# Optimization experiments

Measured on AMD Instinct MI355X. Metric: run time of the kernel, lower is better.

Reference implementation:

```python
import jax, jax.numpy as jnp
import numpy as np

SEQ_LEN = 2048   # configs.seq_len == h == KFSSM H
PRED_LEN = 720   # configs.pred_len == p
D_MODEL = 128    # configs.d_model == KFSSM N (complex state size N//2)
C_OUT = 64       # configs.c_out == channel dim of u
BATCH = 128


def setup_inputs() -> dict:
    key = jax.random.key(0)
    ks = jax.random.split(key, 12)
    H, n2, p = SEQ_LEN, D_MODEL // 2, PRED_LEN
    u = jax.random.normal(ks[0], (BATCH, SEQ_LEN, C_OUT), jnp.float32)
    x_mark_enc = jax.random.normal(ks[1], (BATCH, SEQ_LEN, 4), jnp.float32)
    x_dec = jax.random.normal(ks[2], (BATCH, PRED_LEN, C_OUT), jnp.float32)
    x_mark_dec = jax.random.normal(ks[3], (BATCH, PRED_LEN, 4), jnp.float32)
    # standard-normal noise; scaled by learned std inside reference (matches torch.normal(0, std))
    W_noise = jax.random.normal(ks[4], (BATCH, SEQ_LEN, C_OUT), jnp.float32)
    # Model params
    D = jax.random.normal(ks[5], (H,), jnp.float32)
    log_variance = jnp.log(1.0 + jax.random.uniform(ks[6], (1,), jnp.float32))
    # KFSSM params
    C_param = jax.random.normal(ks[7], (H, n2, 2), jnp.float32)  # view_as_real of complex C
    log_dt = (jax.random.uniform(ks[8], (H,), jnp.float32)
              * (np.log(0.1) - np.log(0.001)) + np.log(0.001))
    log_A_real = jnp.log(0.5 * jnp.ones((H, n2), jnp.float32))
    A_imag = np.pi * jnp.tile(jnp.arange(n2, dtype=jnp.float32)[None, :], (H, 1))
    # outporj: Linear(h -> 2p) then GLU(dim=2)
    proj_w = jax.random.normal(ks[9], (2 * p, H), jnp.float32) * 0.02
    proj_b = jnp.zeros((2 * p,), jnp.float32)
    return dict(u=u, x_mark_enc=x_mark_enc, x_dec=x_dec, x_mark_dec=x_mark_dec,
                W_noise=W_noise, D=D, log_variance=log_variance, C_param=C_param,
                log_dt=log_dt, log_A_real=log_A_real, A_imag=A_imag,
                proj_w=proj_w, proj_b=proj_b)


def _ssm_kernels(Nl, C_param, log_dt, log_A_real, A_imag):
    # KFSSM.forward(N=Nl): returns K, K2 of shape (H, Nl)
    dt = jnp.exp(log_dt)                              # (H,)
    C = C_param[..., 0] + 1j * C_param[..., 1]        # (H, n2)
    A = -jnp.exp(log_A_real) + 1j * A_imag            # (H, n2)
    ar = jnp.arange(Nl, dtype=log_dt.dtype)
    Bk = A[:, :1] * ar[None, :] * dt[:, None]         # (H, Nl) complex
    dtA = A * dt[:, None]                             # (H, n2)
    Kexp = jnp.exp(dtA[:, :, None] * ar[None, None, :])  # (H, n2, Nl)
    Cc = C * (jnp.exp(dtA) - 1.0) / A                 # (H, n2)
    K = 2.0 * jnp.einsum('hn,hnl->hl', Cc, Kexp).real # (H, Nl)
    K2 = 2.0 * (K * Bk).real                          # (H, Nl)
    return K, K2


def reference(u, x_mark_enc, x_dec, x_mark_dec, W_noise, D, log_variance,
              C_param, log_dt, log_A_real, A_imag, proj_w, proj_b):
    # instance normalization over time
    x_mean = jnp.mean(u, axis=1, keepdims=True)                  # (B,1,N)
    u0 = u - x_mean
    x_var = jnp.var(u0, axis=1, ddof=1, keepdims=True) + 1e-5    # unbiased, as torch.var
    un = u0 / jnp.sqrt(x_var)
    # Kalman process noise
    std = jnp.sqrt(jnp.exp(log_variance))                        # (1,)
    W = std * W_noise                                            # (B,L,N)
    l, Nch = un.shape[1], un.shape[2]
    nfft = 2 * l
    K, K2 = _ssm_kernels(Nch, C_param, log_dt, log_A_real, A_imag)  # (H=l, Nch)
    k_f = jnp.fft.rfft(K.T, n=nfft, axis=-1)                     # (Nch, l+1)
    k2_f = jnp.fft.rfft(K2.T, n=nfft, axis=-1)
    u_f = jnp.fft.rfft(jnp.transpose(un, (0, 2, 1)), n=nfft, axis=-1)   # (B,Nch,l+1)
    w_f = jnp.fft.rfft(jnp.transpose(W, (0, 2, 1)), n=nfft, axis=-1)
    y = (jnp.fft.irfft(u_f * k2_f, n=nfft, axis=-1)
         + jnp.fft.irfft(w_f * k_f, n=nfft, axis=-1))            # (B,Nch,2l)
    y = jnp.transpose(y, (0, 2, 1))[:, -l:, :] + un * D[:, None] # (B,l,Nch)
    # outporj: Linear(h->2p) over time axis, then GLU(dim=2); Dropout1d is identity at eval
    z = jnp.einsum('bnh,ph->bnp', jnp.transpose(y, (0, 2, 1)), proj_w) + proj_b  # (B,Nch,2p)
    a, b = jnp.split(z, 2, axis=2)
    y = jnp.transpose(a * jax.nn.sigmoid(b), (0, 2, 1))          # (B,p,Nch)
    y = y * jnp.sqrt(x_var) + x_mean
    return y[:, -PRED_LEN:, :]
```

## Files before the change

kernel.cpp:

```cpp
#include <hip/hip_runtime.h>
#include <math.h>

typedef unsigned short u16;
typedef unsigned int u32;
typedef __attribute__((ext_vector_type(8))) short short8;
typedef __attribute__((ext_vector_type(4))) float f32x4;

#define B_   128
#define L_   2048
#define C_   64
#define P_   720
#define P2_  1440
#define NPAD 1536
#define NFFT 4096
#define NROW (B_*C_)
#define TCHUNK 16

#define PREP_SSMK   512
#define PREP_STATS1 2048
#define PREP_NB     (PREP_SSMK + PREP_STATS1 + 1 + (NPAD * L_) / 256)
#define PF_PACK  4096
#define PF_FFTK  64
#define PF_NB    (PF_PACK + PF_FFTK + 32)

__device__ __forceinline__ u16 f2bf(float f) {
  union { float f; unsigned u; } x; x.f = f;
  unsigned r = x.u + 0x7fffu + ((x.u >> 16) & 1u);
  return (u16)(r >> 16);
}
__device__ __forceinline__ float bf2f_lo(u32 v) {
  union { unsigned u; float f; } x; x.u = v << 16; return x.f;
}
__device__ __forceinline__ float bf2f_hi(u32 v) {
  union { unsigned u; float f; } x; x.u = v & 0xffff0000u; return x.f;
}

__device__ __forceinline__ float2 cmul(float2 a, float2 b) {
  return make_float2(a.x * b.x - a.y * b.y, a.x * b.y + a.y * b.x);
}
__device__ __forceinline__ float2 cadd(float2 a, float2 b) { return make_float2(a.x + b.x, a.y + b.y); }
__device__ __forceinline__ float2 csub(float2 a, float2 b) { return make_float2(a.x - b.x, a.y - b.y); }

#define CSWAP(i, j) { float2 tt = a[i]; a[i] = a[j]; a[j] = tt; }

template<bool INV, bool HZ>
__device__ __forceinline__ void dft16(float2 a[16]) {
  const float S  = INV ? 1.f : -1.f;
  const float c1 = 0.9238795325112867f, s1 = 0.3826834323650898f, q2 = 0.7071067811865476f;
  const float2 W1 = make_float2( c1, S * s1), W2 = make_float2( q2, S * q2), W3 = make_float2( s1, S * c1);
  const float2 W5 = make_float2(-s1, S * c1), W6 = make_float2(-q2, S * q2), W7 = make_float2(-c1, S * s1);
  if (HZ) {
    a[8]  = a[0];
    a[9]  = cmul(a[1], W1);
    a[10] = cmul(a[2], W2);
    a[11] = cmul(a[3], W3);
    a[12] = make_float2(-S * a[4].y, S * a[4].x);
    a[13] = cmul(a[5], W5);
    a[14] = cmul(a[6], W6);
    a[15] = cmul(a[7], W7);
  } else {
    float2 t;
    t = csub(a[0], a[8]);  a[0] = cadd(a[0], a[8]);  a[8]  = t;
    t = csub(a[1], a[9]);  a[1] = cadd(a[1], a[9]);  a[9]  = cmul(t, W1);
    t = csub(a[2], a[10]); a[2] = cadd(a[2], a[10]); a[10] = cmul(t, W2);
    t = csub(a[3], a[11]); a[3] = cadd(a[3], a[11]); a[11] = cmul(t, W3);
    t = csub(a[4], a[12]); a[4] = cadd(a[4], a[12]); a[12] = make_float2(-S * t.y, S * t.x);
    t = csub(a[5], a[13]); a[5] = cadd(a[5], a[13]); a[13] = cmul(t, W5);
    t = csub(a[6], a[14]); a[6] = cadd(a[6], a[14]); a[14] = cmul(t, W6);
    t = csub(a[7], a[15]); a[7] = cadd(a[7], a[15]); a[15] = cmul(t, W7);
  }
#pragma unroll
  for (int h = 0; h < 16; h += 8) {
    float2 t;
    t = csub(a[h+0], a[h+4]); a[h+0] = cadd(a[h+0], a[h+4]); a[h+4] = t;
    t = csub(a[h+1], a[h+5]); a[h+1] = cadd(a[h+1], a[h+5]); a[h+5] = cmul(t, W2);
    t = csub(a[h+2], a[h+6]); a[h+2] = cadd(a[h+2], a[h+6]); a[h+6] = make_float2(-S * t.y, S * t.x);
    t = csub(a[h+3], a[h+7]); a[h+3] = cadd(a[h+3], a[h+7]); a[h+7] = cmul(t, W6);
  }
#pragma unroll
  for (int q = 0; q < 16; q += 4) {
    float2 t;
    t = csub(a[q+0], a[q+2]); a[q+0] = cadd(a[q+0], a[q+2]); a[q+2] = t;
    t = csub(a[q+1], a[q+3]); a[q+1] = cadd(a[q+1], a[q+3]); a[q+3] = make_float2(-S * t.y, S * t.x);
  }
#pragma unroll
  for (int p = 0; p < 16; p += 2) {
    float2 t = csub(a[p], a[p+1]); a[p] = cadd(a[p], a[p+1]); a[p+1] = t;
  }
  CSWAP(1, 8); CSWAP(2, 4); CSWAP(3, 12); CSWAP(5, 10); CSWAP(7, 14); CSWAP(11, 13);
}

__device__ __forceinline__ void twchain(float2 a[16], float2 w1) {
  float2 w2 = cmul(w1, w1);
  float2 w3 = cmul(w2, w1);
  float2 w4 = cmul(w2, w2);
  float2 w5 = cmul(w3, w2);
  float2 w6 = cmul(w3, w3);
  float2 w7 = cmul(w4, w3);
  float2 w8 = cmul(w4, w4);
  float2 w9 = cmul(w5, w4);
  float2 w10 = cmul(w5, w5);
  float2 w11 = cmul(w6, w5);
  float2 w12 = cmul(w6, w6);
  float2 w13 = cmul(w7, w6);
  float2 w14 = cmul(w7, w7);
  float2 w15 = cmul(w8, w7);
  a[1]  = cmul(a[1],  w1);  a[2]  = cmul(a[2],  w2);  a[3]  = cmul(a[3],  w3);
  a[4]  = cmul(a[4],  w4);  a[5]  = cmul(a[5],  w5);  a[6]  = cmul(a[6],  w6);
  a[7]  = cmul(a[7],  w7);  a[8]  = cmul(a[8],  w8);  a[9]  = cmul(a[9],  w9);
  a[10] = cmul(a[10], w10); a[11] = cmul(a[11], w11); a[12] = cmul(a[12], w12);
  a[13] = cmul(a[13], w13); a[14] = cmul(a[14], w14); a[15] = cmul(a[15], w15);
}

__device__ __forceinline__ void lds_wA(float2* X, const float2 r[16], int tid) {
  int base = (tid & 15) * 16 + ((tid >> 4) ^ ((tid & 7) << 1));
#pragma unroll
  for (int i = 0; i < 16; ++i) X[base + i * 256] = r[i];
}
__device__ __forceinline__ void lds_wB(float2* X, const float2 r[16], int tid) {
#pragma unroll
  for (int i = 0; i < 16; ++i)
    X[((tid & 0xF0) + i) * 16 + ((tid & 15) ^ ((i & 7) << 1))] = r[i];
}
__device__ __forceinline__ void lds_rd(const float2* X, float2 r[16], int tid) {
  const float4* X4 = (const float4*)X;
#pragma unroll
  for (int p = 0; p < 8; ++p) {
    float4 v = X4[tid * 8 + (p ^ (tid & 7))];
    r[2 * p]     = make_float2(v.x, v.y);
    r[2 * p + 1] = make_float2(v.z, v.w);
  }
}

__device__ __forceinline__ void fft_fwd_hz(float2 r[16], float2* X, int tid, const float2* twg) {
  dft16<false, true>(r);
  twchain(r, twg[tid]);
  lds_wA(X, r, tid);
  __syncthreads();
  lds_rd(X, r, tid);
  dft16<false, false>(r);
  twchain(r, twg[(tid & 15) << 4]);
  __syncthreads();
  lds_wB(X, r, tid);
  __syncthreads();
  lds_rd(X, r, tid);
  dft16<false, false>(r);
}

__device__ __forceinline__ void fft_inv(float2 r[16], float2* X, int tid, const float2* twg) {
  dft16<true, false>(r);
  __syncthreads();
  lds_wB(X, r, tid);
  __syncthreads();
  lds_rd(X, r, tid);
  float2 wb = twg[(tid & 15) << 4];
  twchain(r, make_float2(wb.x, -wb.y));
  dft16<true, false>(r);
  __syncthreads();
  lds_wA(X, r, tid);
  __syncthreads();
  lds_rd(X, r, tid);
  float2 wa = twg[tid];
  twchain(r, make_float2(wa.x, -wa.y));
  dft16<true, false>(r);
}

__global__ __launch_bounds__(256) void k_prep(const float* __restrict__ pw, u16* __restrict__ wb,
                                              const float* __restrict__ u, float* __restrict__ ps,
                                              float* __restrict__ pq,
                                              const float* __restrict__ Cp, const float* __restrict__ ldt,
                                              const float* __restrict__ lAr, const float* __restrict__ Aim,
                                              float2* __restrict__ kz, float2* __restrict__ tw) {
  __shared__ float4 sb[16][16], qb[16][16];
  int blk = blockIdx.x, tid = threadIdx.x;
  if (blk < PREP_SSMK) {
    int gid = blk * 256 + tid;
    int h = gid & 2047;
    int j = gid >> 11;
    float dt = expf(ldt[h]);
    float accx = 0.f;
    float Ar0 = 0.f;
    for (int n = 0; n < 64; ++n) {
      float Ar = -expf(lAr[h * 64 + n]);
      float Ai = Aim[h * 64 + n];
      if (n == 0) Ar0 = Ar;
      float dAr = Ar * dt, dAi = Ai * dt;
      float er = expf(dAr);
      float s1, c1; sincosf(dAi, &s1, &c1);
      float emr = er * c1 - 1.0f, emi = er * s1;
      float inv = 1.0f / (Ar * Ar + Ai * Ai);
      float qr = (emr * Ar + emi * Ai) * inv;
      float qi = (emi * Ar - emr * Ai) * inv;
      float cr = Cp[(size_t)(h * 64 + n) * 2];
      float ci = Cp[(size_t)(h * 64 + n) * 2 + 1];
      float ccr = cr * qr - ci * qi;
      float cci = cr * qi + ci * qr;
      float ej = expf(dAr * (float)j);
      float sj, cj; sincosf(dAi * (float)j, &sj, &cj);
      accx += ccr * (ej * cj) - cci * (ej * sj);
    }
    float K = 2.0f * accx;
    float K2 = 2.0f * K * (Ar0 * (float)j * dt);
    kz[(size_t)j * L_ + h] = make_float2(K2, -K);
  } else if (blk < PREP_SSMK + PREP_STATS1) {
    int blk2 = blk - PREP_SSMK;
    int b = blk2 >> 4, q = blk2 & 15;
    int c4 = tid & 15, g = tid >> 4;
    const float4* u4 = (const float4*)(u + ((size_t)b * L_ + q * 128) * C_);
    float4 s = make_float4(0.f, 0.f, 0.f, 0.f), sq = s;
#pragma unroll
    for (int i = 0; i < 8; ++i) {
      float4 v = u4[(size_t)(g + 16 * i) * 16 + c4];
      s.x += v.x; s.y += v.y; s.z += v.z; s.w += v.w;
      sq.x += v.x * v.x; sq.y += v.y * v.y; sq.z += v.z * v.z; sq.w += v.w * v.w;
    }
    sb[g][c4] = s; qb[g][c4] = sq;
    __syncthreads();
    if (g == 0) {
      float4 S = sb[0][c4], Q = qb[0][c4];
#pragma unroll
      for (int k = 1; k < 16; ++k) {
        float4 a = sb[k][c4], d = qb[k][c4];
        S.x += a.x; S.y += a.y; S.z += a.z; S.w += a.w;
        Q.x += d.x; Q.y += d.y; Q.z += d.z; Q.w += d.w;
      }
      ((float4*)ps)[blk2 * 16 + c4] = S;
      ((float4*)pq)[blk2 * 16 + c4] = Q;
    }
  } else if (blk == PREP_SSMK + PREP_STATS1) {
    int k = tid;
    double ang = -2.0 * 3.14159265358979323846 * (double)k / 4096.0;
    tw[k] = make_float2((float)cos(ang), (float)sin(ang));
  } else {
    size_t idx = (size_t)(blk - (PREP_SSMK + PREP_STATS1 + 1)) * 256 + tid;
    int n = (int)(idx >> 11);
    int k = (int)(idx & 2047);
    int q = n >> 1;
    float v = 0.f;
    if (q < P_) {
      int p = (n & 1) ? (P_ + q) : q;
      v = pw[(size_t)p * L_ + k];
    }
    wb[idx] = f2bf(v);
  }
}

__global__ __launch_bounds__(256) void k_packfftk(const float* __restrict__ u, const float* __restrict__ Wn,
                                                  const float* __restrict__ lv,
                                                  const float* __restrict__ ps, const float* __restrict__ pq,
                                                  u32* __restrict__ zu,
                                                  const float2* __restrict__ kz, const float2* __restrict__ twg,
                                                  float2* __restrict__ G, float4* __restrict__ mv) {
  __shared__ __align__(16) char smem[33280];
  int blk = blockIdx.x, tid = threadIdx.x;
  if (blk < PF_PACK) {
    int b = blk >> 5;
    int t0 = (blk & 31) << 6;
    float4* mvs = (float4*)smem;
    if (tid < 64) {
      float S = 0.f, Q = 0.f;
#pragma unroll
      for (int q = 0; q < 16; ++q) {
        S += ps[(size_t)(b * 16 + q) * 64 + tid];
        Q += pq[(size_t)(b * 16 + q) * 64 + tid];
      }
      float mean = S * (1.0f / 2048.0f);
      float var = (Q - S * S * (1.0f / 2048.0f)) * (1.0f / 2047.0f) + 1e-5f;
      float sv = sqrtf(var);
      mvs[tid] = make_float4(mean, sv, 1.0f / sv, 0.0f);
    }
    __syncthreads();
    int c = tid & 63, r = tid >> 6;
    float4 m = mvs[c];
    float stdn = sqrtf(__expf(lv[0]));
    __syncthreads();
    float2 (*tile)[65] = (float2(*)[65])smem;
#pragma unroll
    for (int i = 0; i < 16; ++i) {
      int t = t0 + i * 4 + r;
      size_t idx = ((size_t)b * L_ + t) * C_ + c;
      float uu = (u[idx] - m.x) * m.z;
      float ww = Wn[idx] * stdn;
      tile[i * 4 + r][c] = make_float2(uu, ww);
    }
    __syncthreads();
    int t = tid & 63, cb = tid >> 6;
#pragma unroll
    for (int i = 0; i < 16; ++i) {
      int c2 = i * 4 + cb;
      float2 v = tile[t][c2];
      zu[((size_t)(b * C_ + c2)) * L_ + t0 + t] = ((u32)f2bf(v.y) << 16) | (u32)f2bf(v.x);
    }
  } else if (blk < PF_PACK + PF_FFTK) {
    float2* X = (float2*)smem;
    int j = blk - PF_PACK;
    float2 r[16];
#pragma unroll
    for (int n2 = 0; n2 < 8; ++n2) r[n2] = kz[(size_t)j * L_ + n2 * 256 + tid];
    fft_fwd_hz(r, X, tid, twg);
    const float sc = 1.0f / 4096.0f;
#pragma unroll
    for (int k0 = 0; k0 < 16; ++k0)
      G[(size_t)j * NFFT + k0 * 256 + tid] = make_float2(r[k0].x * sc, r[k0].y * sc);
  } else {
    int gid = (blk - (PF_PACK + PF_FFTK)) * 256 + tid;
    int b = gid >> 6, c = gid & 63;
    float S = 0.f, Q = 0.f;
#pragma unroll
    for (int q = 0; q < 16; ++q) {
      S += ps[(size_t)(b * 16 + q) * 64 + c];
      Q += pq[(size_t)(b * 16 + q) * 64 + c];
    }
    float mean = S * (1.0f / 2048.0f);
    float var = (Q - S * S * (1.0f / 2048.0f)) * (1.0f / 2047.0f) + 1e-5f;
    float sv = sqrtf(var);
    mv[gid] = make_float4(mean, sv, 1.0f / sv, 0.0f);
  }
}

__global__ __launch_bounds__(256) void k_fftmain(const u32* __restrict__ zu, const float2* __restrict__ twg,
                                                 const float2* __restrict__ G, const float* __restrict__ Dv,
                                                 u16* __restrict__ yT) {
  __shared__ float2 X[NFFT];
  int row = blockIdx.x;
  int j = row & 63;
  int tid = threadIdx.x;
  float2 r[16];
  float usav[8];
#pragma unroll
  for (int n2 = 0; n2 < 8; ++n2) {
    u32 v = zu[(size_t)row * L_ + n2 * 256 + tid];
    float uu = bf2f_lo(v), ww = bf2f_hi(v);
    r[n2] = make_float2(uu, ww);
    usav[n2] = uu;
  }
  fft_fwd_hz(r, X, tid, twg);
  const float2* Gj = G + (size_t)j * NFFT;
#pragma unroll
  for (int k0 = 0; k0 < 16; ++k0) r[k0] = cmul(r[k0], Gj[k0 * 256 + tid]);
  fft_inv(r, X, tid, twg);
#pragma unroll
  for (int n2 = 8; n2 < 16; ++n2) {
    int t = (n2 - 8) * 256 + tid;
    float yv = r[n2].x + usav[n2 - 8] * Dv[t];
    yT[(size_t)row * L_ + t] = f2bf(yv);
  }
}

__device__ __forceinline__ int lds_ix(int row, int slot) {
  return row * 32 + ((slot ^ ((row >> 1) & 3)) << 3);
}

__global__ __launch_bounds__(256) void k_gemm(const u16* __restrict__ A, const u16* __restrict__ B,
                                              const float* __restrict__ pb, const float4* __restrict__ mv,
                                              float* __restrict__ out) {
  __shared__ u16 As[128 * 32];
  __shared__ u16 Bs[128 * 32];
  __shared__ float ob[32 * 132];
  const int K = L_;
  int tid = threadIdx.x;
  int bid = blockIdx.x;
  int swz = (bid & 7) * 96 + (bid >> 3);
  int bm = swz % 64, bn = swz / 64;
  int wave = tid >> 6, lane = tid & 63;
  int wm = (wave >> 1) << 6, wn = (wave & 1) << 6;
  int lr = lane & 15, lk = lane >> 4;
  int trow = tid >> 2, tslot = tid & 3;
  const u16* Ag = A + (size_t)(bm * 128 + trow) * K + tslot * 8;
  const u16* Bg = B + (size_t)(bn * 128 + trow) * K + tslot * 8;
  f32x4 acc[4][4] = {};
  uint4 pa0 = *(const uint4*)(Ag);
  uint4 pa1 = *(const uint4*)(Ag + (size_t)64 * K);
  uint4 pb0 = *(const uint4*)(Bg);
  uint4 pb1 = *(const uint4*)(Bg + (size_t)64 * K);
  for (int kt = 0; kt < K; kt += 32) {
    __syncthreads();
    *(uint4*)&As[lds_ix(trow, tslot)] = pa0;
    *(uint4*)&As[lds_ix(trow + 64, tslot)] = pa1;
    *(uint4*)&Bs[lds_ix(trow, tslot)] = pb0;
    *(uint4*)&Bs[lds_ix(trow + 64, tslot)] = pb1;
    __syncthreads();
    if (kt + 32 < K) {
      pa0 = *(const uint4*)(Ag + kt + 32);
      pa1 = *(const uint4*)(Ag + (size_t)64 * K + kt + 32);
      pb0 = *(const uint4*)(Bg + kt + 32);
      pb1 = *(const uint4*)(Bg + (size_t)64 * K + kt + 32);
    }
    short8 af[4], bf[4];
#pragma unroll
    for (int i2 = 0; i2 < 4; ++i2) af[i2] = *(const short8*)&As[lds_ix(wm + i2 * 16 + lr, lk)];
#pragma unroll
    for (int j2 = 0; j2 < 4; ++j2) bf[j2] = *(const short8*)&Bs[lds_ix(wn + j2 * 16 + lr, lk)];
#pragma unroll
    for (int i2 = 0; i2 < 4; ++i2)
#pragma unroll
      for (int j2 = 0; j2 < 4; ++j2)
        acc[i2][j2] = __builtin_amdgcn_mfma_f32_16x16x32_bf16(af[i2], bf[j2], acc[i2][j2], 0, 0, 0);
  }
  int col_lo = wn + lr;
  for (int chunk = 0; chunk < 2; ++chunk) {
    __syncthreads();
#pragma unroll
    for (int j2c = 0; j2c < 2; ++j2c) {
      int j2 = chunk * 2 + j2c;
      int col = col_lo + j2 * 16;
      int nglob = bn * 128 + col;
      int q = nglob >> 1;
      float bias = 0.f;
      if (q < P_) bias = pb[(nglob & 1) ? (P_ + q) : q];
      int qloc = col >> 1;
      int s = (qloc & 15) | ((qloc >> 5) << 4);
#pragma unroll
      for (int i2 = 0; i2 < 4; ++i2) {
        int row = wm + i2 * 16 + lk * 4;
        float res[4];
#pragma unroll
        for (int rgi = 0; rgi < 4; ++rgi) {
          float val = acc[i2][j2][rgi] + bias;
          float other = __shfl_xor(val, 1);
          float4 m = mv[bm * 128 + row + rgi];
          res[rgi] = val * (1.0f / (1.0f + __expf(-other))) * m.y + m.x;
        }
        if (!(lane & 1)) {
          *(float4*)&ob[s * 132 + row] = make_float4(res[0], res[1], res[2], res[3]);
        }
      }
    }
    __syncthreads();
    int c = tid & 63, sl4 = tid >> 6;
    for (int rd = 0; rd < 16; ++rd) {
      int slice = rd * 4 + sl4;
      int s = slice >> 1, bb = slice & 1;
      int qloc = (s & 15) + chunk * 16 + ((s >> 4) << 5);
      int qglob = bn * 64 + qloc;
      if (qglob < P_) {
        int bg = bm * 2 + bb;
        out[((size_t)bg * P_ + qglob) * 64 + c] = ob[s * 132 + bb * 64 + c];
      }
    }
  }
}

extern "C" void kernel_launch(void* const* d_in, const int* in_sizes, int n_in,
                              void* d_out, int out_size, void* d_ws, size_t ws_size,
                              hipStream_t stream) {
  const float* u   = (const float*)d_in[0];
  const float* Wn  = (const float*)d_in[4];
  const float* Dv  = (const float*)d_in[5];
  const float* lv  = (const float*)d_in[6];
  const float* Cp  = (const float*)d_in[7];
  const float* ldt = (const float*)d_in[8];
  const float* lAr = (const float*)d_in[9];
  const float* Aim = (const float*)d_in[10];
  const float* pw  = (const float*)d_in[11];
  const float* pb  = (const float*)d_in[12];
  float* out = (float*)d_out;
  char* ws = (char*)d_ws;

  float2* tw = (float2*)(ws + 0);
  float4* mv = (float4*)(ws + (64 << 10));
  float2* G  = (float2*)(ws + (1 << 20));
  float2* kz = (float2*)(ws + (3 << 20));
  u16*    Wb = (u16*)   (ws + (4 << 20));
  float*  ps = (float*) (ws + (10 << 20));
  float*  pq = (float*) (ws + (10 << 20) + (512 << 10));
  u16*    yT = (u16*)   (ws + (16 << 20));
  u32*    zu = (u32*)   (ws + ((size_t)48 << 20));

  k_prep<<<PREP_NB, 256, 0, stream>>>(pw, Wb, u, ps, pq, Cp, ldt, lAr, Aim, kz, tw);
  k_packfftk<<<PF_NB, 256, 0, stream>>>(u, Wn, lv, ps, pq, zu, kz, tw, G, mv);
  k_fftmain<<<NROW, 256, 0, stream>>>(zu, tw, G, Dv, yT);
  k_gemm<<<64 * (NPAD / 128), 256, 0, stream>>>(yT, Wb, pb, mv, out);
}
```

Baseline: 324.9 us.

## Double-buffer GEMM tiles with direct global-to-LDS loads

The bf16 GEMM main loop now loads A and B tiles straight from global memory into LDS with global_load_lds, into two LDS buffers. The XOR swizzle is applied by choosing a permuted source column instead of permuting the LDS destination. The loop waits on vmcnt and a raw s_barrier, computes from the current buffer, then issues the loads for the tile two steps ahead into the buffer it just freed. This removes the register staging copy and one sync per iteration, and overlaps loads with MFMA work. The cost is double the LDS for tiles, which can lower occupancy, and reliance on hand-written waitcnt ordering.

```diff
diff --git a/kernel.cpp b/kernel.cpp
--- a/kernel.cpp
+++ b/kernel.cpp
@@ -22,6 +22,10 @@
 #define PF_PACK  4096
 #define PF_FFTK  64
 #define PF_NB    (PF_PACK + PF_FFTK + 32)
+
+#define GLOAD_LDS16(g, l) __builtin_amdgcn_global_load_lds( \
+    (const __attribute__((address_space(1))) unsigned int*)(g), \
+    (__attribute__((address_space(3))) unsigned int*)(l), 16, 0, 0)
 
 __device__ __forceinline__ u16 f2bf(float f) {
   union { float f; unsigned u; } x; x.f = f;
@@ -354,8 +358,8 @@
 __global__ __launch_bounds__(256) void k_gemm(const u16* __restrict__ A, const u16* __restrict__ B,
                                               const float* __restrict__ pb, const float4* __restrict__ mv,
                                               float* __restrict__ out) {
-  __shared__ u16 As[128 * 32];
-  __shared__ u16 Bs[128 * 32];
+  __shared__ u16 As[2][128 * 32];
+  __shared__ u16 Bs[2][128 * 32];
   __shared__ float ob[32 * 132];
   const int K = L_;
   int tid = threadIdx.x;
@@ -365,37 +369,47 @@
   int wave = tid >> 6, lane = tid & 63;
   int wm = (wave >> 1) << 6, wn = (wave & 1) << 6;
   int lr = lane & 15, lk = lane >> 4;
-  int trow = tid >> 2, tslot = tid & 3;
-  const u16* Ag = A + (size_t)(bm * 128 + trow) * K + tslot * 8;
-  const u16* Bg = B + (size_t)(bn * 128 + trow) * K + tslot * 8;
+  int srow = wave * 32 + (lane >> 2);
+  int sslot = lane & 3;
+  int scol = (sslot ^ ((srow >> 1) & 3)) << 3;
+  const u16* Ag = A + (size_t)(bm * 128 + srow) * K + scol;
+  const u16* Bg = B + (size_t)(bn * 128 + srow) * K + scol;
+  int woff = wave * 32 * 32;
   f32x4 acc[4][4] = {};
-  uint4 pa0 = *(const uint4*)(Ag);
-  uint4 pa1 = *(const uint4*)(Ag + (size_t)64 * K);
-  uint4 pb0 = *(const uint4*)(Bg);
-  uint4 pb1 = *(const uint4*)(Bg + (size_t)64 * K);
+  GLOAD_LDS16(Ag, &As[0][woff]);
+  GLOAD_LDS16(Ag + (size_t)16 * K, &As[0][woff + 16 * 32]);
+  GLOAD_LDS16(Bg, &Bs[0][woff]);
+  GLOAD_LDS16(Bg + (size_t)16 * K, &Bs[0][woff + 16 * 32]);
+  GLOAD_LDS16(Ag + 32, &As[1][woff]);
+  GLOAD_LDS16(Ag + 32 + (size_t)16 * K, &As[1][woff + 16 * 32]);
+  GLOAD_LDS16(Bg + 32, &Bs[1][woff]);
+  GLOAD_LDS16(Bg + 32 + (size_t)16 * K, &Bs[1][woff + 16 * 32]);
+  int cur = 0;
   for (int kt = 0; kt < K; kt += 32) {
-    __syncthreads();
-    *(uint4*)&As[lds_ix(trow, tslot)] = pa0;
-    *(uint4*)&As[lds_ix(trow + 64, tslot)] = pa1;
-    *(uint4*)&Bs[lds_ix(trow, tslot)] = pb0;
-    *(uint4*)&Bs[lds_ix(trow + 64, tslot)] = pb1;
-    __syncthreads();
     if (kt + 32 < K) {
-      pa0 = *(const uint4*)(Ag + kt + 32);
-      pa1 = *(const uint4*)(Ag + (size_t)64 * K + kt + 32);
-      pb0 = *(const uint4*)(Bg + kt + 32);
-      pb1 = *(const uint4*)(Bg + (size_t)64 * K + kt + 32);
-    }
+      asm volatile("s_waitcnt vmcnt(4)" ::: "memory");
+    } else {
+      asm volatile("s_waitcnt vmcnt(0)" ::: "memory");
+    }
+    __builtin_amdgcn_s_barrier();
     short8 af[4], bf[4];
 #pragma unroll
-    for (int i2 = 0; i2 < 4; ++i2) af[i2] = *(const short8*)&As[lds_ix(wm + i2 * 16 + lr, lk)];
-#pragma unroll
-    for (int j2 = 0; j2 < 4; ++j2) bf[j2] = *(const short8*)&Bs[lds_ix(wn + j2 * 16 + lr, lk)];
+    for (int i2 = 0; i2 < 4; ++i2) af[i2] = *(const short8*)&As[cur][lds_ix(wm + i2 * 16 + lr, lk)];
+#pragma unroll
+    for (int j2 = 0; j2 < 4; ++j2) bf[j2] = *(const short8*)&Bs[cur][lds_ix(wn + j2 * 16 + lr, lk)];
 #pragma unroll
     for (int i2 = 0; i2 < 4; ++i2)
 #pragma unroll
       for (int j2 = 0; j2 < 4; ++j2)
         acc[i2][j2] = __builtin_amdgcn_mfma_f32_16x16x32_bf16(af[i2], bf[j2], acc[i2][j2], 0, 0, 0);
+    __builtin_amdgcn_s_barrier();
+    if (kt + 64 < K) {
+      GLOAD_LDS16(Ag + kt + 64, &As[cur][woff]);
+      GLOAD_LDS16(Ag + kt + 64 + (size_t)16 * K, &As[cur][woff + 16 * 32]);
+      GLOAD_LDS16(Bg + kt + 64, &Bs[cur][woff]);
+      GLOAD_LDS16(Bg + kt + 64 + (size_t)16 * K, &Bs[cur][woff + 16 * 32]);
+    }
+    cur ^= 1;
   }
   int col_lo = wn + lr;
   for (int chunk = 0; chunk < 2; ++chunk) {
```

Result: no change. 328.0 us (+0.9%).
